# Optimization experiments

Hardware: AMD Instinct MI355X
Metric: run time of the kernel (lower is better)

Reference implementation:

```python
import jax, jax.numpy as jnp
import numpy as np
import math

N_HEADS = 32
N_KV_HEADS = 8
MAX_SEQ_LEN = 2048


def _rope_cos_sin(seq_len, head_dim, dtype):
    # precompute_freqs_cis: theta=10000, positions 0..seq_len-1 (note: NOT offset by start_pos, faithful to source)
    inv_freq = 1.0 / (10000.0 ** (jnp.arange(0, head_dim, 2, dtype=jnp.float32) / head_dim))
    t = jnp.arange(seq_len, dtype=jnp.float32)
    angles = jnp.outer(t, inv_freq)  # [S, hd/2]
    return jnp.cos(angles).astype(dtype), jnp.sin(angles).astype(dtype)


def _apply_rope(x, cos, sin):
    # x: [B, S, H, hd]; rotate consecutive pairs (llama complex convention)
    B, S, H, hd = x.shape
    xr = x.reshape(B, S, H, hd // 2, 2)
    x1, x2 = xr[..., 0], xr[..., 1]
    c = cos[None, :, None, :]
    s = sin[None, :, None, :]
    o1 = x1 * c - x2 * s
    o2 = x1 * s + x2 * c
    return jnp.stack([o1, o2], axis=-1).reshape(B, S, H, hd)


def setup_inputs() -> dict:
    key = jax.random.key(0)
    ks = jax.random.split(key, 5)
    dim = 4096
    B, S = 1, 2048
    sd = 1.0 / math.sqrt(dim)
    return {
        "x": jax.random.normal(ks[0], (B, S, dim), dtype=jnp.float32),
        "wq": jax.random.normal(ks[1], (4096, 4096), dtype=jnp.float32) * sd,
        "wk": jax.random.normal(ks[2], (1024, 4096), dtype=jnp.float32) * sd,
        "wv": jax.random.normal(ks[3], (1024, 4096), dtype=jnp.float32) * sd,
        "wo": jax.random.normal(ks[4], (4096, 4096), dtype=jnp.float32) * sd,
        "start_pos": 0,
    }


def reference(x, wq, wk, wv, wo, start_pos):
    B, S, D = x.shape
    Hq, Hkv = N_HEADS, N_KV_HEADS
    hd = D // Hq
    n_rep = Hq // Hkv

    xq = (x @ wq.T).reshape(B, S, Hq, hd)
    xk = (x @ wk.T).reshape(B, S, Hkv, hd)
    xv = (x @ wv.T).reshape(B, S, Hkv, hd)

    cos, sin = _rope_cos_sin(S, hd, x.dtype)
    xq = _apply_rope(xq, cos, sin)
    xk = _apply_rope(xk, cos, sin)

    # KV cache append + read back [:, :start_pos+S] (start_pos is a static Python int)
    cache_k = jnp.zeros((B, MAX_SEQ_LEN, Hkv, hd), dtype=x.dtype)
    cache_v = jnp.zeros((B, MAX_SEQ_LEN, Hkv, hd), dtype=x.dtype)
    cache_k = jax.lax.dynamic_update_slice(cache_k, xk, (0, start_pos, 0, 0))
    cache_v = jax.lax.dynamic_update_slice(cache_v, xv, (0, start_pos, 0, 0))
    kv_len = start_pos + S
    keys = cache_k[:, :kv_len]    # [B, K, Hkv, hd]
    values = cache_v[:, :kv_len]

    # GQA repeat_kv: [B, K, Hkv, hd] -> [B, K, Hq, hd]
    keys = jnp.broadcast_to(keys[:, :, :, None, :], (B, kv_len, Hkv, n_rep, hd)).reshape(B, kv_len, Hq, hd)
    values = jnp.broadcast_to(values[:, :, :, None, :], (B, kv_len, Hkv, n_rep, hd)).reshape(B, kv_len, Hq, hd)

    scale = 1.0 / math.sqrt(hd)
    scores = jnp.einsum('bqhd,bkhd->bhqk', xq, keys) * scale  # [B, Hq, S, K]
    # NOTE: source applies NO causal mask — faithful reproduction
    attn = jax.nn.softmax(scores, axis=-1)
    out = jnp.einsum('bhqk,bkhd->bqhd', attn, values).reshape(B, S, Hq * hd)
    return out @ wo.T
```

## Files before the change

### kernel.cpp

```cpp
#include <hip/hip_runtime.h>
#include <hip/hip_bf16.h>

typedef _Float16 f16_t;
typedef unsigned int uint;
typedef __attribute__((ext_vector_type(8))) _Float16 f16x8;
typedef __attribute__((ext_vector_type(4))) _Float16 f16x4;
typedef __attribute__((ext_vector_type(4))) float f32x4;
typedef __attribute__((ext_vector_type(16))) float f32x16;

__global__ __launch_bounds__(256) void repack_x16(const float* __restrict__ src,
                                                  uint16_t* __restrict__ dh)
{
    const int p  = blockIdx.y;
    const int kb = blockIdx.x;
    const int tid = threadIdx.x;
    const int rr = tid >> 3;
    const int k4 = tid & 7;
    const int slot = k4 >> 1;
    const int so   = (k4 & 1) * 4;
    uint16_t* bh = dh + ((size_t)p * 128 + kb) * 4096;
    #pragma unroll
    for (int it = 0; it < 4; ++it) {
        const int r = it * 32 + rr;
        const float4 v = *reinterpret_cast<const float4*>(
            &src[((size_t)p * 128 + r) * 4096 + kb * 32 + k4 * 4]);
        float f[4] = {v.x, v.y, v.z, v.w};
        f16x4 h;
        #pragma unroll
        for (int e = 0; e < 4; ++e) h[e] = (f16_t)f[e];
        const int pos = r * 32 + ((slot ^ ((r >> 1) & 3)) << 3) + so;
        *reinterpret_cast<f16x4*>(&bh[pos]) = h;
    }
}

__global__ __launch_bounds__(256) void repack_w96_16(const float* __restrict__ wq,
                                                     const float* __restrict__ wk,
                                                     const float* __restrict__ wv,
                                                     uint16_t* __restrict__ dst)
{
    const int kb  = blockIdx.x;
    const int pan = blockIdx.y;
    const int tid = threadIdx.x;
    const int k4 = tid & 7;
    const int slot = k4 >> 1;
    const int so   = (k4 & 1) * 4;
    uint16_t* bh = dst + ((size_t)pan * 128 + kb) * 3072;
    #pragma unroll
    for (int it = 0; it < 3; ++it) {
        const int r = it * 32 + (tid >> 3);
        const int n = pan * 96 + r;
        const float* srow = (n < 4096) ? (wq + (size_t)n * 4096)
                          : (n < 5120) ? (wk + (size_t)(n - 4096) * 4096)
                                       : (wv + (size_t)(n - 5120) * 4096);
        const float4 v = *reinterpret_cast<const float4*>(srow + kb * 32 + k4 * 4);
        float f[4] = {v.x, v.y, v.z, v.w};
        f16x4 h;
        #pragma unroll
        for (int e = 0; e < 4; ++e) h[e] = (f16_t)f[e];
        const int pos = r * 32 + ((slot ^ ((r >> 1) & 3)) << 3) + so;
        *reinterpret_cast<f16x4*>(&bh[pos]) = h;
    }
}

__global__ __launch_bounds__(256) void repack_h16(const float* __restrict__ src,
                                                  uint16_t* __restrict__ dh)
{
    const int p  = blockIdx.y;
    const int kb = blockIdx.x;
    const int tid = threadIdx.x;
    const int rr = tid >> 3;
    const int k4 = tid & 7;
    const int slot = k4 >> 1;
    const int so   = (k4 & 1) * 4;
    uint16_t* bh = dh + ((size_t)p * 128 + kb) * 4096;
    #pragma unroll
    for (int it = 0; it < 4; ++it) {
        const int r = it * 32 + rr;
        const float4 v = *reinterpret_cast<const float4*>(
            &src[((size_t)p * 128 + r) * 4096 + kb * 32 + k4 * 4]);
        float f[4] = {v.x, v.y, v.z, v.w};
        f16x4 h;
        #pragma unroll
        for (int e = 0; e < 4; ++e) h[e] = (f16_t)f[e];
        const int pos = r * 32 + ((slot ^ ((r >> 1) & 3)) << 3) + so;
        *reinterpret_cast<f16x4*>(&bh[pos]) = h;
    }
}

__global__ __launch_bounds__(512) void gemm_qkv9(const uint16_t* __restrict__ xh,
                                                 const uint16_t* __restrict__ wqkv,
                                                 float* __restrict__ xq,
                                                 float* __restrict__ xk,
                                                 float* __restrict__ xv)
{
    __shared__ char lds[2][40960];

    const int bid = blockIdx.x;
    const int swz = (bid & 7) * 64 + (bid >> 3);
    const int by = swz >> 5;
    const int bx = swz & 31;
    const int tid = threadIdx.x;
    const int w = tid >> 6, lane = tid & 63;
    const int wm = w >> 2, wn = w & 3;
    const int fr = lane & 15, s4 = lane >> 4;

    const uint16_t* sp[5];
    int dof[5];
    int stridec[5];
    #pragma unroll
    for (int i = 0; i < 5; ++i) {
        const int c = w + 8 * i;
        if (c < 16) {
            const int kk = c >> 3, inner = c & 7;
            sp[i] = xh + (size_t)by * 524288 + kk * 4096 + inner * 512 + lane * 8;
            dof[i] = c * 1024;
            stridec[i] = 8192;
        } else {
            const int cb = c - 16;
            const int pan = cb / 12, rem = cb % 12;
            const int kk = rem / 6, inner = rem % 6;
            sp[i] = wqkv + (size_t)(bx * 2 + pan) * 393216 + kk * 3072 + inner * 512 + lane * 8;
            dof[i] = 16384 + cb * 1024;
            stridec[i] = 6144;
        }
    }

    f32x4 acc[4][3] = {};

    #pragma unroll
    for (int i = 0; i < 5; ++i)
        __builtin_amdgcn_global_load_lds(
            (const __attribute__((address_space(1))) void*)(sp[i]),
            (__attribute__((address_space(3))) void*)(&lds[0][0] + dof[i]), 16, 0, 0);
    asm volatile("s_waitcnt vmcnt(0)" ::: "memory");
    __builtin_amdgcn_s_barrier();
    __builtin_amdgcn_sched_barrier(0);

    for (int t = 0; t < 64; ++t) {
        const char* b = &lds[t & 1][0];
        if (t + 1 < 64) {
            char* nb = &lds[(t + 1) & 1][0];
            #pragma unroll
            for (int i = 0; i < 5; ++i)
                __builtin_amdgcn_global_load_lds(
                    (const __attribute__((address_space(1))) void*)(sp[i] + (size_t)(t + 1) * stridec[i]),
                    (__attribute__((address_space(3))) void*)(nb + dof[i]), 16, 0, 0);
        }
        #pragma unroll
        for (int kk = 0; kk < 2; ++kk) {
            f16x8 fb[3];
            #pragma unroll
            for (int j = 0; j < 3; ++j) {
                const int cbp = wn * 48 + j * 16 + fr;
                const int pan = (cbp >= 96) ? 1 : 0;
                const int rb = cbp - pan * 96;
                fb[j] = *reinterpret_cast<const f16x8*>(
                    b + 16384 + pan * 12288 + kk * 6144 + rb * 64 + ((s4 ^ ((rb >> 1) & 3)) << 4));
            }
            #pragma unroll
            for (int ri = 0; ri < 4; ++ri) {
                const int rloc = wm * 64 + ri * 16 + fr;
                f16x8 fh = *reinterpret_cast<const f16x8*>(
                    b + kk * 8192 + rloc * 64 + ((s4 ^ ((rloc >> 1) & 3)) << 4));
                __builtin_amdgcn_s_setprio(1);
                #pragma unroll
                for (int j = 0; j < 3; ++j)
                    acc[ri][j] = __builtin_amdgcn_mfma_f32_16x16x32_f16(fh, fb[j], acc[ri][j], 0, 0, 0);
                __builtin_amdgcn_s_setprio(0);
            }
        }
        asm volatile("s_waitcnt vmcnt(0)" ::: "memory");
        __builtin_amdgcn_s_barrier();
        __builtin_amdgcn_sched_barrier(0);
    }

    const int r0 = by * 128 + wm * 64 + s4 * 4;
    const int c0 = bx * 192 + wn * 48 + fr;
    #pragma unroll
    for (int ri = 0; ri < 4; ++ri)
        #pragma unroll
        for (int j = 0; j < 3; ++j) {
            const int col = c0 + j * 16;
            #pragma unroll
            for (int rr = 0; rr < 4; ++rr) {
                const int row = r0 + ri * 16 + rr;
                if (col < 4096)      xq[(size_t)row * 4096 + col] = acc[ri][j][rr];
                else if (col < 5120) xk[(size_t)row * 1024 + (col - 4096)] = acc[ri][j][rr];
                else                 xv[(size_t)row * 1024 + (col - 5120)] = acc[ri][j][rr];
            }
        }
}

__global__ __launch_bounds__(512) void gemm_out9(const uint16_t* __restrict__ aoh,
                                                 const uint16_t* __restrict__ woh,
                                                 float* __restrict__ out)
{
    __shared__ char lds[2][32768];

    const int bid = blockIdx.x;
    const int swz = (bid & 7) * 64 + (bid >> 3);
    const int by = swz >> 5;
    const int bx = swz & 31;
    const int tid = threadIdx.x;
    const int w = tid >> 6, lane = tid & 63;
    const int wm = w >> 2, wn = w & 3;
    const int fr = lane & 15, s4 = lane >> 4;

    const uint16_t* sp[4];
    int dof[4];
    #pragma unroll
    for (int i = 0; i < 4; ++i) {
        const int c = w + 8 * i;
        if (c < 16) {
            const int kk = c >> 3, inner = c & 7;
            sp[i] = aoh + (size_t)by * 524288 + kk * 4096 + inner * 512 + lane * 8;
            dof[i] = c * 1024;
        } else {
            const int cb = c - 16;
            const int kk = cb >> 3, inner = cb & 7;
            sp[i] = woh + (size_t)bx * 524288 + kk * 4096 + inner * 512 + lane * 8;
            dof[i] = 16384 + cb * 1024;
        }
    }

    f32x4 acc[4][2] = {};

    #pragma unroll
    for (int i = 0; i < 4; ++i)
        __builtin_amdgcn_global_load_lds(
            (const __attribute__((address_space(1))) void*)(sp[i]),
            (__attribute__((address_space(3))) void*)(&lds[0][0] + dof[i]), 16, 0, 0);
    asm volatile("s_waitcnt vmcnt(0)" ::: "memory");
    __builtin_amdgcn_s_barrier();
    __builtin_amdgcn_sched_barrier(0);

    for (int t = 0; t < 64; ++t) {
        const char* b = &lds[t & 1][0];
        if (t + 1 < 64) {
            char* nb = &lds[(t + 1) & 1][0];
            #pragma unroll
            for (int i = 0; i < 4; ++i)
                __builtin_amdgcn_global_load_lds(
                    (const __attribute__((address_space(1))) void*)(sp[i] + (size_t)(t + 1) * 8192),
                    (__attribute__((address_space(3))) void*)(nb + dof[i]), 16, 0, 0);
        }
        #pragma unroll
        for (int kk = 0; kk < 2; ++kk) {
            f16x8 fb[2];
            #pragma unroll
            for (int j = 0; j < 2; ++j) {
                const int cbp = wn * 32 + j * 16 + fr;
                fb[j] = *reinterpret_cast<const f16x8*>(
                    b + 16384 + kk * 8192 + cbp * 64 + ((s4 ^ ((cbp >> 1) & 3)) << 4));
            }
            #pragma unroll
            for (int ri = 0; ri < 4; ++ri) {
                const int rloc = wm * 64 + ri * 16 + fr;
                f16x8 fh = *reinterpret_cast<const f16x8*>(
                    b + kk * 8192 + rloc * 64 + ((s4 ^ ((rloc >> 1) & 3)) << 4));
                __builtin_amdgcn_s_setprio(1);
                #pragma unroll
                for (int j = 0; j < 2; ++j)
                    acc[ri][j] = __builtin_amdgcn_mfma_f32_16x16x32_f16(fh, fb[j], acc[ri][j], 0, 0, 0);
                __builtin_amdgcn_s_setprio(0);
            }
        }
        asm volatile("s_waitcnt vmcnt(0)" ::: "memory");
        __builtin_amdgcn_s_barrier();
        __builtin_amdgcn_sched_barrier(0);
    }

    const int r0 = by * 128 + wm * 64 + s4 * 4;
    const int c0 = bx * 128 + wn * 32 + fr;
    #pragma unroll
    for (int ri = 0; ri < 4; ++ri)
        #pragma unroll
        for (int j = 0; j < 2; ++j)
            #pragma unroll
            for (int rr = 0; rr < 4; ++rr)
                out[(size_t)(r0 + ri * 16 + rr) * 4096 + c0 + j * 16] = acc[ri][j][rr];
}

__global__ __launch_bounds__(256) void rope_k(float* __restrict__ xq, float* __restrict__ xk)
{
    const int idx = blockIdx.x * 256 + threadIdx.x;
    const int TOTQ = 2048 * 32 * 64;
    int s, j;
    float* base;
    bool isq = idx < TOTQ;
    if (isq) {
        s = idx >> 11;
        const int rem = idx & 2047;
        j = rem & 63;
        base = xq + (size_t)s * 4096 + (rem >> 6) * 128 + 2 * j;
    } else {
        const int i2 = idx - TOTQ;
        s = i2 >> 9;
        const int rem = i2 & 511;
        j = rem & 63;
        base = xk + (size_t)s * 1024 + (rem >> 6) * 128 + 2 * j;
    }
    const float invf = exp2f(-(float)j * (13.287712379549449f / 64.0f));
    const float ang = (float)s * invf;
    float sn, cs;
    sincosf(ang, &sn, &cs);
    float2 v = *reinterpret_cast<float2*>(base);
    float2 r;
    r.x = v.x * cs - v.y * sn;
    r.y = v.x * sn + v.y * cs;
    if (isq) { r.x *= 0.08838834764831845f; r.y *= 0.08838834764831845f; }
    *reinterpret_cast<float2*>(base) = r;
}

__global__ __launch_bounds__(256) void conv_kv(const float* __restrict__ xk,
                                               const float* __restrict__ xv,
                                               uint16_t* __restrict__ kvg)
{
    __shared__ float V[32][129];
    const int t = blockIdx.x;
    const int h = blockIdx.y;
    const int tid = threadIdx.x;
    uint16_t* tile = kvg + ((size_t)(h * 64 + t)) * 8192;

    #pragma unroll
    for (int i = 0; i < 4; ++i) {
        int v = i * 256 + tid;
        int row = v >> 5, c4 = (v & 31) * 4;
        *reinterpret_cast<float4*>(&V[row][c4]) =
            *reinterpret_cast<const float4*>(&xv[(size_t)(t * 32 + row) * 1024 + h * 128 + c4]);
    }

    {
        const int r = tid >> 3;
        const int d0 = (tid & 7) * 16;
        float f[16];
        const float* kr = &xk[(size_t)(t * 32 + r) * 1024 + h * 128 + d0];
        *reinterpret_cast<float4*>(&f[0])  = *reinterpret_cast<const float4*>(kr);
        *reinterpret_cast<float4*>(&f[4])  = *reinterpret_cast<const float4*>(kr + 4);
        *reinterpret_cast<float4*>(&f[8])  = *reinterpret_cast<const float4*>(kr + 8);
        *reinterpret_cast<float4*>(&f[12]) = *reinterpret_cast<const float4*>(kr + 12);
        #pragma unroll
        for (int cc = 0; cc < 2; ++cc) {
            f16x8 hv;
            #pragma unroll
            for (int e = 0; e < 8; ++e) hv[e] = (f16_t)f[cc * 8 + e];
            const int c = (d0 >> 3) + cc;
            const int pos = r * 128 + ((c ^ (r & 15)) << 3);
            *reinterpret_cast<f16x8*>(&tile[pos]) = hv;
        }
    }
    __syncthreads();
    {
        const int d = tid >> 1;
        const int k0 = (tid & 1) * 16;
        float g[16];
        #pragma unroll
        for (int j = 0; j < 16; ++j) g[j] = V[k0 + j][d];
        #pragma unroll
        for (int cc = 0; cc < 2; ++cc) {
            f16x8 hv;
            #pragma unroll
            for (int e = 0; e < 8; ++e) hv[e] = (f16_t)g[cc * 8 + e];
            const int c = (k0 >> 3) + cc;
            const int pos = 4096 + d * 32 + ((c ^ (d & 3)) << 3);
            *reinterpret_cast<f16x8*>(&tile[pos]) = hv;
        }
    }
}

__device__ __forceinline__ uint cvtpkh(float lo, float hi) {
    uint r;
    asm("v_cvt_pkrtz_f16_f32 %0, %1, %2" : "=v"(r) : "v"(lo), "v"(hi));
    return r;
}
__device__ __forceinline__ void permswap(uint& a, uint& b) {
    asm("v_permlane32_swap_b32 %0, %1" : "+v"(a), "+v"(b));
}
__device__ __forceinline__ f16x8 pack4h(uint w0, uint w1, uint w2, uint w3) {
    union { uint u[4]; f16x8 v; } t;
    t.u[0] = w0; t.u[1] = w1; t.u[2] = w2; t.u[3] = w3;
    return t.v;
}

__global__ __launch_bounds__(512, 2) void attn_mfma(const float* __restrict__ xq,
                                                    const uint16_t* __restrict__ kvg,
                                                    uint16_t* __restrict__ aoh)
{
    __shared__ char lds[2][16384];

    const int b = blockIdx.x;
    const int kvh = b & 7;
    const int r = b >> 3;
    const int h = kvh * 4 + (r & 3);
    const int q0 = (r >> 2) * 256;
    const int tid = threadIdx.x;
    const int w = tid >> 6;
    const int lane = tid & 63;
    const int ln31 = lane & 31;
    const int hi = lane >> 5;

    const int q = q0 + w * 32 + ln31;
    const float* qrow = xq + (size_t)q * 4096 + h * 128;
    f16x8 Qh[8];
    #pragma unroll
    for (int ks = 0; ks < 8; ++ks) {
        float f[8];
        *reinterpret_cast<float4*>(&f[0]) = *reinterpret_cast<const float4*>(qrow + ks * 16 + hi * 8);
        *reinterpret_cast<float4*>(&f[4]) = *reinterpret_cast<const float4*>(qrow + ks * 16 + hi * 8 + 4);
        #pragma unroll
        for (int e = 0; e < 8; ++e) Qh[ks][e] = (f16_t)f[e];
    }

    const char* gkv = (const char*)kvg + (size_t)kvh * 64 * 16384;

    f32x16 oacc[4] = {{}, {}, {}, {}};
    float m = -3.0e38f, l = 0.f;

    {
        #pragma unroll
        for (int i = 0; i < 2; ++i) {
            const int chunk = i * 8 + w;
            __builtin_amdgcn_global_load_lds(
                (const __attribute__((address_space(1))) void*)(gkv + chunk * 1024 + lane * 16),
                (__attribute__((address_space(3))) void*)(&lds[0][chunk * 1024]),
                16, 0, 0);
        }
    }

    for (int t = 0; t < 64; ++t) {
        __syncthreads();
        if (t + 1 < 64) {
            const char* g = gkv + (size_t)(t + 1) * 16384;
            const int buf = (t + 1) & 1;
            #pragma unroll
            for (int i = 0; i < 2; ++i) {
                const int chunk = i * 8 + w;
                __builtin_amdgcn_global_load_lds(
                    (const __attribute__((address_space(1))) void*)(g + chunk * 1024 + lane * 16),
                    (__attribute__((address_space(3))) void*)(&lds[buf][chunk * 1024]),
                    16, 0, 0);
            }
        }
        const int cur = t & 1;
        const char* Kf = lds[cur];
        const char* Vf = lds[cur] + 8192;

        f32x16 s0 = {}, s1 = {};
        __builtin_amdgcn_s_setprio(1);
        #pragma unroll
        for (int ks = 0; ks < 8; ++ks) {
            const int byt = ln31 * 256 + ((ks * 32 + hi * 16) ^ ((ln31 & 15) << 4));
            f16x8 a = *reinterpret_cast<const f16x8*>(Kf + byt);
            if (ks & 1) s1 = __builtin_amdgcn_mfma_f32_32x32x16_f16(a, Qh[ks], s1, 0, 0, 0);
            else        s0 = __builtin_amdgcn_mfma_f32_32x32x16_f16(a, Qh[ks], s0, 0, 0, 0);
        }
        __builtin_amdgcn_s_setprio(0);
        f32x16 s = s0 + s1;

        float pmax = s[0];
        #pragma unroll
        for (int jj = 1; jj < 16; ++jj) pmax = fmaxf(pmax, s[jj]);
        pmax = fmaxf(pmax, __shfl_xor(pmax, 32));
        if (!__all(pmax - m <= 8.0f)) {
            const float mnew = fmaxf(m, pmax);
            const float corr = __expf(m - mnew);
            l *= corr;
            #pragma unroll
            for (int dt = 0; dt < 4; ++dt) oacc[dt] *= corr;
            m = mnew;
        }
        float psum = 0.f;
        #pragma unroll
        for (int jj = 0; jj < 16; ++jj) {
            float pv = __expf(s[jj] - m);
            s[jj] = pv;
            psum += pv;
        }
        psum += __shfl_xor(psum, 32);
        l += psum;

        #pragma unroll
        for (int ks = 0; ks < 2; ++ks) {
            const int b0 = ks * 8;
            uint wa = cvtpkh(s[b0 + 0], s[b0 + 1]);
            uint wb = cvtpkh(s[b0 + 2], s[b0 + 3]);
            uint wc = cvtpkh(s[b0 + 4], s[b0 + 5]);
            uint wd = cvtpkh(s[b0 + 6], s[b0 + 7]);
            permswap(wa, wc); permswap(wb, wd);
            f16x8 Pf = pack4h(wa, wb, wc, wd);
            __builtin_amdgcn_s_setprio(1);
            #pragma unroll
            for (int dt = 0; dt < 4; ++dt) {
                const int row = dt * 32 + ln31;
                const int byt = row * 64 + ((ks * 32 + hi * 16) ^ ((row & 3) << 4));
                f16x8 vh = *reinterpret_cast<const f16x8*>(Vf + byt);
                oacc[dt] = __builtin_amdgcn_mfma_f32_32x32x16_f16(vh, Pf, oacc[dt], 0, 0, 0);
            }
            __builtin_amdgcn_s_setprio(0);
        }
    }

    const float invl = 1.0f / l;
    const int p   = q >> 7;
    const int rr_ = q & 127;
    const int rsw = (rr_ >> 1) & 3;
    #pragma unroll
    for (int dt = 0; dt < 4; ++dt) {
        const int kb = h * 4 + dt;
        uint16_t* bh = aoh + ((size_t)p * 128 + kb) * 4096;
        #pragma unroll
        for (int g4 = 0; g4 < 4; ++g4) {
            f16x4 hv;
            #pragma unroll
            for (int e = 0; e < 4; ++e)
                hv[e] = (f16_t)(oacc[dt][g4 * 4 + e] * invl);
            const int pos = rr_ * 32 + ((g4 ^ rsw) << 3) + 4 * hi;
            *reinterpret_cast<f16x4*>(&bh[pos]) = hv;
        }
    }
}

extern "C" void kernel_launch(void* const* d_in, const int* in_sizes, int n_in,
                              void* d_out, int out_size, void* d_ws, size_t ws_size,
                              hipStream_t stream)
{
    const float* x  = (const float*)d_in[0];
    const float* wq = (const float*)d_in[1];
    const float* wk = (const float*)d_in[2];
    const float* wv = (const float*)d_in[3];
    const float* wo = (const float*)d_in[4];
    float* out = (float*)d_out;

    float* ws = (float*)d_ws;
    float*    xq   = ws;
    uint16_t* kvg  = (uint16_t*)(ws + 8388608);
    float*    xk   = ws + 12582912;
    float*    xv   = ws + 14680064;
    uint16_t* aoh  = (uint16_t*)(ws + 12582912);
    uint16_t* xh   = (uint16_t*)(ws + 20971520);
    uint16_t* wqkv = (uint16_t*)(ws + 29360128);
    uint16_t* woh  = (uint16_t*)(ws + 41943040);

    dim3 blk(256);
    repack_x16   <<<dim3(128, 16), blk, 0, stream>>>(x, xh);
    repack_w96_16<<<dim3(128, 64), blk, 0, stream>>>(wq, wk, wv, wqkv);
    gemm_qkv9    <<<dim3(512), dim3(512), 0, stream>>>(xh, wqkv, xq, xk, xv);
    repack_h16   <<<dim3(128, 32), blk, 0, stream>>>(wo, woh);
    rope_k       <<<dim3(20480), blk, 0, stream>>>(xq, xk);
    conv_kv      <<<dim3(64, 8), blk, 0, stream>>>(xk, xv, kvg);
    attn_mfma    <<<dim3(256), dim3(512), 0, stream>>>(xq, kvg, aoh);
    gemm_out9    <<<dim3(512), dim3(512), 0, stream>>>(aoh, woh, out);
}
```

Measured before the change: 386.2 us.

## Store QKV in fp16, fuse RoPE into consumers, enlarge output GEMM tile

The QKV GEMM epilogue now writes fp16 instead of fp32. The separate rope_k pass is removed: RoPE for K is applied in conv_kv, and RoPE plus the softmax scale for Q is applied when attention loads Q. The output projection GEMM moves to 256x128 tiles, so it launches 256 blocks with larger LDS buffers. This removes a full read-modify-write pass over Q and K, halves the intermediate traffic, and raises data reuse in the last GEMM. The cost is rounding pre-RoPE values to fp16, using the fast __sincosf, and possibly lower occupancy in the larger GEMM.

```diff
diff --git a/kernel.cpp b/kernel.cpp
--- a/kernel.cpp
+++ b/kernel.cpp
@@ -7,6 +7,8 @@
 typedef __attribute__((ext_vector_type(4))) _Float16 f16x4;
 typedef __attribute__((ext_vector_type(4))) float f32x4;
 typedef __attribute__((ext_vector_type(16))) float f32x16;
+
+#define ROPE_C (13.287712379549449f / 64.0f)
 
 __global__ __launch_bounds__(256) void repack_x16(const float* __restrict__ src,
                                                   uint16_t* __restrict__ dh)
@@ -89,9 +91,9 @@
 
 __global__ __launch_bounds__(512) void gemm_qkv9(const uint16_t* __restrict__ xh,
                                                  const uint16_t* __restrict__ wqkv,
-                                                 float* __restrict__ xq,
-                                                 float* __restrict__ xk,
-                                                 float* __restrict__ xv)
+                                                 uint16_t* __restrict__ xq16,
+                                                 uint16_t* __restrict__ xk16,
+                                                 uint16_t* __restrict__ xv16)
 {
     __shared__ char lds[2][40960];
 
@@ -184,21 +186,24 @@
             #pragma unroll
             for (int rr = 0; rr < 4; ++rr) {
                 const int row = r0 + ri * 16 + rr;
-                if (col < 4096)      xq[(size_t)row * 4096 + col] = acc[ri][j][rr];
-                else if (col < 5120) xk[(size_t)row * 1024 + (col - 4096)] = acc[ri][j][rr];
-                else                 xv[(size_t)row * 1024 + (col - 5120)] = acc[ri][j][rr];
-            }
-        }
-}
-
-__global__ __launch_bounds__(512) void gemm_out9(const uint16_t* __restrict__ aoh,
+                const f16_t v = (f16_t)acc[ri][j][rr];
+                uint16_t bits;
+                __builtin_memcpy(&bits, &v, 2);
+                if (col < 4096)      xq16[(size_t)row * 4096 + col] = bits;
+                else if (col < 5120) xk16[(size_t)row * 1024 + (col - 4096)] = bits;
+                else                 xv16[(size_t)row * 1024 + (col - 5120)] = bits;
+            }
+        }
+}
+
+__global__ __launch_bounds__(512) void gemm_out8(const uint16_t* __restrict__ aoh,
                                                  const uint16_t* __restrict__ woh,
                                                  float* __restrict__ out)
 {
-    __shared__ char lds[2][32768];
+    __shared__ char lds[2][49152];
 
     const int bid = blockIdx.x;
-    const int swz = (bid & 7) * 64 + (bid >> 3);
+    const int swz = (bid & 7) * 32 + (bid >> 3);
     const int by = swz >> 5;
     const int bx = swz & 31;
     const int tid = threadIdx.x;
@@ -206,27 +211,25 @@
     const int wm = w >> 2, wn = w & 3;
     const int fr = lane & 15, s4 = lane >> 4;
 
-    const uint16_t* sp[4];
-    int dof[4];
-    #pragma unroll
-    for (int i = 0; i < 4; ++i) {
+    const uint16_t* sp[6];
+    int dof[6];
+    #pragma unroll
+    for (int i = 0; i < 6; ++i) {
         const int c = w + 8 * i;
-        if (c < 16) {
-            const int kk = c >> 3, inner = c & 7;
-            sp[i] = aoh + (size_t)by * 524288 + kk * 4096 + inner * 512 + lane * 8;
+        if (c < 32) {
+            const int pan = c >> 4, sub = c & 15;
+            sp[i] = aoh + (size_t)(2 * by + pan) * 524288 + sub * 512 + lane * 8;
             dof[i] = c * 1024;
         } else {
-            const int cb = c - 16;
-            const int kk = cb >> 3, inner = cb & 7;
-            sp[i] = woh + (size_t)bx * 524288 + kk * 4096 + inner * 512 + lane * 8;
-            dof[i] = 16384 + cb * 1024;
-        }
-    }
-
-    f32x4 acc[4][2] = {};
-
-    #pragma unroll
-    for (int i = 0; i < 4; ++i)
+            sp[i] = woh + (size_t)bx * 524288 + (c - 32) * 512 + lane * 8;
+            dof[i] = 32768 + (c - 32) * 1024;
+        }
+    }
+
+    f32x4 acc[8][2] = {};
+
+    #pragma unroll
+    for (int i = 0; i < 6; ++i)
         __builtin_amdgcn_global_load_lds(
             (const __attribute__((address_space(1))) void*)(sp[i]),
             (__attribute__((address_space(3))) void*)(&lds[0][0] + dof[i]), 16, 0, 0);
@@ -239,7 +242,7 @@
         if (t + 1 < 64) {
             char* nb = &lds[(t + 1) & 1][0];
             #pragma unroll
-            for (int i = 0; i < 4; ++i)
+            for (int i = 0; i < 6; ++i)
                 __builtin_amdgcn_global_load_lds(
                     (const __attribute__((address_space(1))) void*)(sp[i] + (size_t)(t + 1) * 8192),
                     (__attribute__((address_space(3))) void*)(nb + dof[i]), 16, 0, 0);
@@ -251,17 +254,23 @@
             for (int j = 0; j < 2; ++j) {
                 const int cbp = wn * 32 + j * 16 + fr;
                 fb[j] = *reinterpret_cast<const f16x8*>(
-                    b + 16384 + kk * 8192 + cbp * 64 + ((s4 ^ ((cbp >> 1) & 3)) << 4));
-            }
-            #pragma unroll
-            for (int ri = 0; ri < 4; ++ri) {
-                const int rloc = wm * 64 + ri * 16 + fr;
-                f16x8 fh = *reinterpret_cast<const f16x8*>(
-                    b + kk * 8192 + rloc * 64 + ((s4 ^ ((rloc >> 1) & 3)) << 4));
+                    b + 32768 + kk * 8192 + cbp * 64 + ((s4 ^ ((cbp >> 1) & 3)) << 4));
+            }
+            #pragma unroll
+            for (int p = 0; p < 4; ++p) {
+                f16x8 fh[2];
+                #pragma unroll
+                for (int f = 0; f < 2; ++f) {
+                    const int rloc = p * 32 + f * 16 + fr;
+                    fh[f] = *reinterpret_cast<const f16x8*>(
+                        b + wm * 16384 + kk * 8192 + rloc * 64 + ((s4 ^ ((rloc >> 1) & 3)) << 4));
+                }
                 __builtin_amdgcn_s_setprio(1);
                 #pragma unroll
-                for (int j = 0; j < 2; ++j)
-                    acc[ri][j] = __builtin_amdgcn_mfma_f32_16x16x32_f16(fh, fb[j], acc[ri][j], 0, 0, 0);
+                for (int f = 0; f < 2; ++f)
+                    #pragma unroll
+                    for (int j = 0; j < 2; ++j)
+                        acc[p * 2 + f][j] = __builtin_amdgcn_mfma_f32_16x16x32_f16(fh[f], fb[j], acc[p * 2 + f][j], 0, 0, 0);
                 __builtin_amdgcn_s_setprio(0);
             }
         }
@@ -270,10 +279,10 @@
         __builtin_amdgcn_sched_barrier(0);
     }
 
-    const int r0 = by * 128 + wm * 64 + s4 * 4;
+    const int r0 = by * 256 + wm * 128 + s4 * 4;
     const int c0 = bx * 128 + wn * 32 + fr;
     #pragma unroll
-    for (int ri = 0; ri < 4; ++ri)
+    for (int ri = 0; ri < 8; ++ri)
         #pragma unroll
         for (int j = 0; j < 2; ++j)
             #pragma unroll
@@ -281,39 +290,8 @@
                 out[(size_t)(r0 + ri * 16 + rr) * 4096 + c0 + j * 16] = acc[ri][j][rr];
 }
 
-__global__ __launch_bounds__(256) void rope_k(float* __restrict__ xq, float* __restrict__ xk)
-{
-    const int idx = blockIdx.x * 256 + threadIdx.x;
-    const int TOTQ = 2048 * 32 * 64;
-    int s, j;
-    float* base;
-    bool isq = idx < TOTQ;
-    if (isq) {
-        s = idx >> 11;
-        const int rem = idx & 2047;
-        j = rem & 63;
-        base = xq + (size_t)s * 4096 + (rem >> 6) * 128 + 2 * j;
-    } else {
-        const int i2 = idx - TOTQ;
-        s = i2 >> 9;
-        const int rem = i2 & 511;
-        j = rem & 63;
-        base = xk + (size_t)s * 1024 + (rem >> 6) * 128 + 2 * j;
-    }
-    const float invf = exp2f(-(float)j * (13.287712379549449f / 64.0f));
-    const float ang = (float)s * invf;
-    float sn, cs;
-    sincosf(ang, &sn, &cs);
-    float2 v = *reinterpret_cast<float2*>(base);
-    float2 r;
-    r.x = v.x * cs - v.y * sn;
-    r.y = v.x * sn + v.y * cs;
-    if (isq) { r.x *= 0.08838834764831845f; r.y *= 0.08838834764831845f; }
-    *reinterpret_cast<float2*>(base) = r;
-}
-
-__global__ __launch_bounds__(256) void conv_kv(const float* __restrict__ xk,
-                                               const float* __restrict__ xv,
+__global__ __launch_bounds__(256) void conv_kv(const uint16_t* __restrict__ xk16,
+                                               const uint16_t* __restrict__ xv16,
                                                uint16_t* __restrict__ kvg)
 {
     __shared__ float V[32][129];
@@ -324,21 +302,34 @@
 
     #pragma unroll
     for (int i = 0; i < 4; ++i) {
-        int v = i * 256 + tid;
-        int row = v >> 5, c4 = (v & 31) * 4;
-        *reinterpret_cast<float4*>(&V[row][c4]) =
-            *reinterpret_cast<const float4*>(&xv[(size_t)(t * 32 + row) * 1024 + h * 128 + c4]);
+        const int v = i * 256 + tid;
+        const int row = v >> 5, c4 = (v & 31) * 4;
+        f16x4 hv = *reinterpret_cast<const f16x4*>(&xv16[(size_t)(t * 32 + row) * 1024 + h * 128 + c4]);
+        #pragma unroll
+        for (int e = 0; e < 4; ++e) V[row][c4 + e] = (float)hv[e];
     }
 
     {
         const int r = tid >> 3;
         const int d0 = (tid & 7) * 16;
+        const int pos_ = t * 32 + r;
         float f[16];
-        const float* kr = &xk[(size_t)(t * 32 + r) * 1024 + h * 128 + d0];
-        *reinterpret_cast<float4*>(&f[0])  = *reinterpret_cast<const float4*>(kr);
-        *reinterpret_cast<float4*>(&f[4])  = *reinterpret_cast<const float4*>(kr + 4);
-        *reinterpret_cast<float4*>(&f[8])  = *reinterpret_cast<const float4*>(kr + 8);
-        *reinterpret_cast<float4*>(&f[12]) = *reinterpret_cast<const float4*>(kr + 12);
+        const uint16_t* kr = &xk16[(size_t)pos_ * 1024 + h * 128 + d0];
+        f16x8 k0 = *reinterpret_cast<const f16x8*>(kr);
+        f16x8 k1 = *reinterpret_cast<const f16x8*>(kr + 8);
+        #pragma unroll
+        for (int e = 0; e < 8; ++e) { f[e] = (float)k0[e]; f[8 + e] = (float)k1[e]; }
+        #pragma unroll
+        for (int i = 0; i < 8; ++i) {
+            const int j = (d0 >> 1) + i;
+            const float invf = exp2f(-(float)j * ROPE_C);
+            const float ang = (float)pos_ * invf;
+            float sn, cs;
+            __sincosf(ang, &sn, &cs);
+            const float x1 = f[2 * i], x2 = f[2 * i + 1];
+            f[2 * i]     = x1 * cs - x2 * sn;
+            f[2 * i + 1] = x1 * sn + x2 * cs;
+        }
         #pragma unroll
         for (int cc = 0; cc < 2; ++cc) {
             f16x8 hv;
@@ -382,7 +373,7 @@
     return t.v;
 }
 
-__global__ __launch_bounds__(512, 2) void attn_mfma(const float* __restrict__ xq,
+__global__ __launch_bounds__(512, 2) void attn_mfma(const uint16_t* __restrict__ xq16,
                                                     const uint16_t* __restrict__ kvg,
                                                     uint16_t* __restrict__ aoh)
 {
@@ -400,13 +391,26 @@
     const int hi = lane >> 5;
 
     const int q = q0 + w * 32 + ln31;
-    const float* qrow = xq + (size_t)q * 4096 + h * 128;
+    const uint16_t* qrow = xq16 + (size_t)q * 4096 + h * 128;
     f16x8 Qh[8];
     #pragma unroll
     for (int ks = 0; ks < 8; ++ks) {
+        const int dbase = ks * 16 + hi * 8;
+        f16x8 raw = *reinterpret_cast<const f16x8*>(qrow + dbase);
         float f[8];
-        *reinterpret_cast<float4*>(&f[0]) = *reinterpret_cast<const float4*>(qrow + ks * 16 + hi * 8);
-        *reinterpret_cast<float4*>(&f[4]) = *reinterpret_cast<const float4*>(qrow + ks * 16 + hi * 8 + 4);
+        #pragma unroll
+        for (int e = 0; e < 8; ++e) f[e] = (float)raw[e];
+        #pragma unroll
+        for (int i = 0; i < 4; ++i) {
+            const int j = (dbase >> 1) + i;
+            const float invf = exp2f(-(float)j * ROPE_C);
+            const float ang = (float)q * invf;
+            float sn, cs;
+            __sincosf(ang, &sn, &cs);
+            const float x1 = f[2 * i], x2 = f[2 * i + 1];
+            f[2 * i]     = (x1 * cs - x2 * sn) * 0.08838834764831845f;
+            f[2 * i + 1] = (x1 * sn + x2 * cs) * 0.08838834764831845f;
+        }
         #pragma unroll
         for (int e = 0; e < 8; ++e) Qh[ks][e] = (f16_t)f[e];
     }
@@ -532,10 +536,10 @@
     float* out = (float*)d_out;
 
     float* ws = (float*)d_ws;
-    float*    xq   = ws;
+    uint16_t* xq16 = (uint16_t*)ws;
     uint16_t* kvg  = (uint16_t*)(ws + 8388608);
-    float*    xk   = ws + 12582912;
-    float*    xv   = ws + 14680064;
+    uint16_t* xk16 = (uint16_t*)(ws + 12582912);
+    uint16_t* xv16 = (uint16_t*)(ws + 14680064);
     uint16_t* aoh  = (uint16_t*)(ws + 12582912);
     uint16_t* xh   = (uint16_t*)(ws + 20971520);
     uint16_t* wqkv = (uint16_t*)(ws + 29360128);
@@ -544,10 +548,9 @@
     dim3 blk(256);
     repack_x16   <<<dim3(128, 16), blk, 0, stream>>>(x, xh);
     repack_w96_16<<<dim3(128, 64), blk, 0, stream>>>(wq, wk, wv, wqkv);
-    gemm_qkv9    <<<dim3(512), dim3(512), 0, stream>>>(xh, wqkv, xq, xk, xv);
+    gemm_qkv9    <<<dim3(512), dim3(512), 0, stream>>>(xh, wqkv, xq16, xk16, xv16);
     repack_h16   <<<dim3(128, 32), blk, 0, stream>>>(wo, woh);
-    rope_k       <<<dim3(20480), blk, 0, stream>>>(xq, xk);
-    conv_kv      <<<dim3(64, 8), blk, 0, stream>>>(xk, xv, kvg);
-    attn_mfma    <<<dim3(256), dim3(512), 0, stream>>>(xq, kvg, aoh);
-    gemm_out9    <<<dim3(512), dim3(512), 0, stream>>>(aoh, woh, out);
-}
+    conv_kv      <<<dim3(64, 8), blk, 0, stream>>>(xk16, xv16, kvg);
+    attn_mfma    <<<dim3(256), dim3(512), 0, stream>>>(xq16, kvg, aoh);
+    gemm_out8    <<<dim3(256), dim3(512), 0, stream>>>(aoh, woh, out);
+}
```

Measured after the change: 366.3 us. 1.05x faster.
